# Kernel optimization log

Hardware: AMD Instinct MI355X
Metric: run time of the kernel (lower is better)

## Reference

```python
import jax, jax.numpy as jnp
import numpy as np

B, N, D_IN, D_H, D_OUT = 2, 512, 128, 128, 128


def _mlp2(x, W1, b1, W2, b2):
    # Linear -> SiLU -> Linear
    h = jax.nn.silu(x @ W1 + b1)
    return h @ W2 + b2


def _safe_norm(d2):
    # norm with zero (not NaN) gradient at 0, matching torch.norm's subgradient
    pos = d2 > 0
    return jnp.where(pos, jnp.sqrt(jnp.where(pos, d2, 1.0)), 0.0)


def setup_inputs() -> dict:
    key = jax.random.key(0)
    ks = jax.random.split(key, 16)

    def lin(k, fan_in, fan_out):
        bound = 1.0 / np.sqrt(fan_in)
        kw, kb = jax.random.split(k)
        W = jax.random.uniform(kw, (fan_in, fan_out), jnp.float32, -bound, bound)
        b = jax.random.uniform(kb, (fan_out,), jnp.float32, -bound, bound)
        return W, b

    Ws1, bs1 = lin(ks[0], D_IN, D_H)
    Ws2, bs2 = lin(ks[1], D_H, D_OUT)
    Wv1, bv1 = lin(ks[2], D_IN, D_H)
    Wv2, bv2 = lin(ks[3], D_H, D_OUT)
    Wa1, ba1 = lin(ks[4], D_IN + 3, D_H)
    Wa2, ba2 = lin(ks[5], D_H, 1)

    node_features = jax.random.normal(ks[6], (B, N, D_IN), jnp.float32)
    coordinates = jax.random.normal(ks[7], (B, N, 3), jnp.float32)
    edge_mask = jax.random.randint(ks[8], (B, N, N), 0, 2, jnp.int32)

    return dict(node_features=node_features, coordinates=coordinates, edge_mask=edge_mask,
                Ws1=Ws1, bs1=bs1, Ws2=Ws2, bs2=bs2,
                Wv1=Wv1, bv1=bv1, Wv2=Wv2, bv2=bv2,
                Wa1=Wa1, ba1=ba1, Wa2=Wa2, ba2=ba2)


def reference(node_features, coordinates, edge_mask,
              Ws1, bs1, Ws2, bs2, Wv1, bv1, Wv2, bv2, Wa1, ba1, Wa2, ba2):
    num_atoms = node_features.shape[1]

    # pairwise geometry: diff[b,i,j,:] = x_i - x_j
    diff = coordinates[:, :, None, :] - coordinates[:, None, :, :]  # [B,N,N,3]
    d2 = jnp.sum(diff * diff, axis=-1)
    distances = _safe_norm(d2)  # [B,N,N]

    # per-node scalar branch
    scalar_features = _mlp2(node_features, Ws1, bs1, Ws2, bs2)  # [B,N,D_OUT]

    # radial features + broadcast node features -> attention MLP
    dist_features = jnp.stack(
        [distances, 1.0 / (distances + 1e-6), jnp.exp(-distances)], axis=-1)  # [B,N,N,3]
    nf_exp = jnp.broadcast_to(node_features[:, :, None, :],
                              node_features.shape[:2] + (num_atoms, node_features.shape[-1]))
    attention_input = jnp.concatenate([nf_exp, dist_features], axis=-1)  # [B,N,N,D_IN+3]
    attn_logits = _mlp2(attention_input, Wa1, ba1, Wa2, ba2)[..., 0]  # [B,N,N]

    attn_logits = jnp.where(edge_mask != 0, attn_logits, -jnp.inf)
    attention_weights = jax.nn.softmax(attn_logits, axis=-1)  # [B,N,N]

    # direction-weighted aggregation
    vector_aggregated = jnp.einsum('bijc,bij->bic', diff, attention_weights)  # [B,N,3]

    vector_features = _mlp2(node_features, Wv1, bv1, Wv2, bv2)  # [B,N,D_OUT]
    vector_out = vector_aggregated * vector_features[..., :3]  # [B,N,3]

    return scalar_features, vector_out
```

## Files before the change

kernel.cpp:

```cpp
#include <hip/hip_runtime.h>
#include <math.h>

#define NB 2
#define NN 512
#define DD 128
#define LOG2E 1.4426950408889634f

typedef unsigned long long ull;

__device__ __forceinline__ float exp2_hw(float x) {
    float r; asm("v_exp_f32 %0, %1" : "=v"(r) : "v"(x)); return r;
}
__device__ __forceinline__ float silu_f(float x) {
    float e = exp2_hw(-LOG2E * x);
    return x * __builtin_amdgcn_rcpf(1.0f + e);
}

#define UPD(P, Ae, ff1, ff2, ff3, accv)                                       \
    { float pre = fmaf(ff3, P.w, fmaf(ff2, P.z, fmaf(ff1, P.y, P.x)));        \
      float e   = exp2_hw(pre);                                               \
      float rc  = __builtin_amdgcn_rcpf(1.0f + e);                            \
      accv      = fmaf(pre * Ae, rc, accv); }

__global__ __launch_bounds__(256) void k_all(
    const float* __restrict__ nf,
    const float* __restrict__ coords,
    const int*   __restrict__ mask,
    const float* __restrict__ Ws1, const float* __restrict__ bs1,
    const float* __restrict__ Ws2, const float* __restrict__ bs2,
    const float* __restrict__ Wv1, const float* __restrict__ bv1,
    const float* __restrict__ Wv2, const float* __restrict__ bv2,
    const float* __restrict__ Wa1, const float* __restrict__ ba1,
    const float* __restrict__ Wa2, const float* __restrict__ ba2p,
    float* __restrict__ scalar_out,
    float* __restrict__ vec_out)
{
    __shared__ __align__(16) float s_nf[DD];
    __shared__ __align__(16) float s_hs[DD];
    __shared__ __align__(16) float s_hv[DD];
    __shared__ __align__(16) float s_am[DD];
    __shared__ float  s_part[3][256];
    __shared__ float4 s_pk[DD];
    __shared__ short  s_act[NN];
    __shared__ int    s_cnt8[8], s_off8[8], s_nactS;
    __shared__ float  s_red[4], s_red2[4][4];

    const int row  = blockIdx.x;
    const int b    = row >> 9;
    const int tid  = threadIdx.x;
    const int lane = tid & 63;
    const int wid  = tid >> 6;
    const int c    = tid & 127;
    const int h    = tid >> 7;

    if (tid < DD) s_nf[tid] = nf[row * DD + tid];
    const int* mrow = mask + (size_t)row * NN;
    const bool m0 = (mrow[tid]       != 0);
    const bool m1 = (mrow[tid + 256] != 0);
    const ull  bal0 = __ballot(m0);
    const ull  bal1 = __ballot(m1);
    if (lane == 0) {
        s_cnt8[wid]     = __popcll(bal0);
        s_cnt8[4 + wid] = __popcll(bal1);
    }
    __syncthreads();

    if (tid == 0) {
        int a = 0;
        #pragma unroll
        for (int q = 0; q < 8; ++q) { s_off8[q] = a; a += s_cnt8[q]; }
        s_nactS = a;
    }
    {
        float ps = 0.f, pv = 0.f, pa = 0.f;
        const float4* nf4 = (const float4*)s_nf;
        const int kq0 = h * 16;
        #pragma unroll 4
        for (int kk = 0; kk < 16; ++kk) {
            float4 x = nf4[kq0 + kk];
            const int k = (kq0 + kk) * 4;
            ps = fmaf(x.x, Ws1[(k+0)*DD + c], ps);
            ps = fmaf(x.y, Ws1[(k+1)*DD + c], ps);
            ps = fmaf(x.z, Ws1[(k+2)*DD + c], ps);
            ps = fmaf(x.w, Ws1[(k+3)*DD + c], ps);
            pv = fmaf(x.x, Wv1[(k+0)*DD + c], pv);
            pv = fmaf(x.y, Wv1[(k+1)*DD + c], pv);
            pv = fmaf(x.z, Wv1[(k+2)*DD + c], pv);
            pv = fmaf(x.w, Wv1[(k+3)*DD + c], pv);
            pa = fmaf(x.x, Wa1[(k+0)*DD + c], pa);
            pa = fmaf(x.y, Wa1[(k+1)*DD + c], pa);
            pa = fmaf(x.z, Wa1[(k+2)*DD + c], pa);
            pa = fmaf(x.w, Wa1[(k+3)*DD + c], pa);
        }
        s_part[0][tid] = ps;
        s_part[1][tid] = pv;
        s_part[2][tid] = pa;
    }
    __syncthreads();

    if (tid < DD) {
        s_hs[tid] = silu_f(s_part[0][tid] + s_part[0][128 + tid] + bs1[tid]);
        s_hv[tid] = silu_f(s_part[1][tid] + s_part[1][128 + tid] + bv1[tid]);
        float base = s_part[2][tid] + s_part[2][128 + tid] + ba1[tid];
        float4 p;
        p.x = -LOG2E * base;
        p.y = -LOG2E * Wa1[128 * DD + tid];
        p.z = -LOG2E * Wa1[129 * DD + tid];
        p.w = -LOG2E * Wa1[130 * DD + tid];
        s_pk[tid] = p;
        s_am[tid] = -Wa2[tid];
    }
    {
        const ull lm = (1ull << lane) - 1ull;
        if (m0) s_act[s_off8[wid]     + __popcll(bal0 & lm)] = (short)tid;
        if (m1) s_act[s_off8[4 + wid] + __popcll(bal1 & lm)] = (short)(tid + 256);
    }
    __syncthreads();

    {
        float pb = 0.f;
        const float4* hs4 = (const float4*)s_hs;
        const int kq0 = h * 16;
        #pragma unroll 4
        for (int kk = 0; kk < 16; ++kk) {
            float4 x = hs4[kq0 + kk];
            const int k = (kq0 + kk) * 4;
            pb = fmaf(x.x, Ws2[(k+0)*DD + c], pb);
            pb = fmaf(x.y, Ws2[(k+1)*DD + c], pb);
            pb = fmaf(x.z, Ws2[(k+2)*DD + c], pb);
            pb = fmaf(x.w, Ws2[(k+3)*DD + c], pb);
        }
        s_part[0][tid] = pb;
    }
    if (tid >= 128 && tid < 224) {
        const int idx = tid - 128;
        const int col = idx >> 5;
        const int kq  = idx & 31;
        float vp = 0.f;
        #pragma unroll
        for (int u = 0; u < 4; ++u) {
            const int k = 4 * kq + u;
            vp = fmaf(s_hv[k], Wv2[k * DD + col], vp);
        }
        s_part[1][tid] = vp;
    }

    const int nact = __builtin_amdgcn_readfirstlane(s_nactS);
    const bool act0 = (tid < nact);
    const bool act1 = (tid + 256 < nact);
    const bool w_has1 = ((tid & ~63) + 256) < nact;

    const float ba2l = ba2p[0] * LOG2E;
    const float xi0 = coords[row * 3 + 0];
    const float xi1 = coords[row * 3 + 1];
    const float xi2 = coords[row * 3 + 2];
    const float* cb = coords + (size_t)b * NN * 3;

    float dx0 = 0.f, dy0 = 0.f, dz0 = 0.f, f1_0 = 0.f, f2_0 = 0.f, f3_0 = 0.f;
    float dx1 = 0.f, dy1 = 0.f, dz1 = 0.f, f1_1 = 0.f, f2_1 = 0.f, f3_1 = 0.f;
    float acc0 = ba2l, acc1 = ba2l;

    {
        const int j = ((int)s_act[act0 ? tid : 0]) & (NN - 1);
        dx0 = xi0 - cb[j * 3 + 0];
        dy0 = xi1 - cb[j * 3 + 1];
        dz0 = xi2 - cb[j * 3 + 2];
        float d2 = fmaf(dx0, dx0, fmaf(dy0, dy0, dz0 * dz0));
        float d  = sqrtf(d2);
        f1_0 = d;
        float x  = d + 1e-6f;
        float rc = __builtin_amdgcn_rcpf(x);
        f2_0 = rc * fmaf(-x, rc, 2.0f);
        f3_0 = exp2_hw(-LOG2E * d);
    }
    if (w_has1) {
        const int j = ((int)s_act[act1 ? tid + 256 : 0]) & (NN - 1);
        dx1 = xi0 - cb[j * 3 + 0];
        dy1 = xi1 - cb[j * 3 + 1];
        dz1 = xi2 - cb[j * 3 + 2];
        float d2 = fmaf(dx1, dx1, fmaf(dy1, dy1, dz1 * dz1));
        float d  = sqrtf(d2);
        f1_1 = d;
        float x  = d + 1e-6f;
        float rc = __builtin_amdgcn_rcpf(x);
        f2_1 = rc * fmaf(-x, rc, 2.0f);
        f3_1 = exp2_hw(-LOG2E * d);
    }

    const float4* A4 = (const float4*)s_am;
    for (int t4 = 0; t4 < DD / 4; ++t4) {
        float4 A  = A4[t4];
        float4 P0 = s_pk[4 * t4 + 0];
        float4 P1 = s_pk[4 * t4 + 1];
        float4 P2 = s_pk[4 * t4 + 2];
        float4 P3 = s_pk[4 * t4 + 3];
        UPD(P0, A.x, f1_0, f2_0, f3_0, acc0);
        UPD(P1, A.y, f1_0, f2_0, f3_0, acc0);
        UPD(P2, A.z, f1_0, f2_0, f3_0, acc0);
        UPD(P3, A.w, f1_0, f2_0, f3_0, acc0);
        if (w_has1) {
            UPD(P0, A.x, f1_1, f2_1, f3_1, acc1);
            UPD(P1, A.y, f1_1, f2_1, f3_1, acc1);
            UPD(P2, A.z, f1_1, f2_1, f3_1, acc1);
            UPD(P3, A.w, f1_1, f2_1, f3_1, acc1);
        }
    }
    __syncthreads();

    if (tid < DD) {
        scalar_out[row * DD + tid] = s_part[0][tid] + s_part[0][128 + tid] + bs2[tid];
    }
    float vf_col = 0.f;
    if (tid < 3) {
        float v = bv2[tid];
        const float* pp = &s_part[1][128 + tid * 32];
        for (int r = 0; r < 32; ++r) v += pp[r];
        vf_col = v;
    }

    float mloc = -__builtin_inff();
    if (act0) mloc = acc0;
    if (act1) mloc = fmaxf(mloc, acc1);
    #pragma unroll
    for (int ofs = 32; ofs >= 1; ofs >>= 1) mloc = fmaxf(mloc, __shfl_xor(mloc, ofs));
    if (lane == 0) s_red[wid] = mloc;
    __syncthreads();
    const float mx = fmaxf(fmaxf(s_red[0], s_red[1]), fmaxf(s_red[2], s_red[3]));

    float es = 0.f, wx = 0.f, wy = 0.f, wz = 0.f;
    if (act0) {
        float e = exp2_hw(acc0 - mx);
        es += e; wx = fmaf(e, dx0, wx); wy = fmaf(e, dy0, wy); wz = fmaf(e, dz0, wz);
    }
    if (w_has1 && act1) {
        float e = exp2_hw(acc1 - mx);
        es += e; wx = fmaf(e, dx1, wx); wy = fmaf(e, dy1, wy); wz = fmaf(e, dz1, wz);
    }
    #pragma unroll
    for (int ofs = 32; ofs >= 1; ofs >>= 1) {
        es += __shfl_xor(es, ofs);
        wx += __shfl_xor(wx, ofs);
        wy += __shfl_xor(wy, ofs);
        wz += __shfl_xor(wz, ofs);
    }
    if (lane == 0) {
        s_red2[wid][0] = es; s_red2[wid][1] = wx;
        s_red2[wid][2] = wy; s_red2[wid][3] = wz;
    }
    __syncthreads();

    if (tid < 3) {
        float tot = s_red2[0][0] + s_red2[1][0] + s_red2[2][0] + s_red2[3][0];
        float num = s_red2[0][1+tid] + s_red2[1][1+tid] + s_red2[2][1+tid] + s_red2[3][1+tid];
        vec_out[row * 3 + tid] = (num / tot) * vf_col;
    }
}

extern "C" void kernel_launch(void* const* d_in, const int* in_sizes, int n_in,
                              void* d_out, int out_size, void* d_ws, size_t ws_size,
                              hipStream_t stream) {
    const float* nf     = (const float*)d_in[0];
    const float* coords = (const float*)d_in[1];
    const int*   mask   = (const int*)  d_in[2];
    const float* Ws1 = (const float*)d_in[3];  const float* bs1 = (const float*)d_in[4];
    const float* Ws2 = (const float*)d_in[5];  const float* bs2 = (const float*)d_in[6];
    const float* Wv1 = (const float*)d_in[7];  const float* bv1 = (const float*)d_in[8];
    const float* Wv2 = (const float*)d_in[9];  const float* bv2 = (const float*)d_in[10];
    const float* Wa1 = (const float*)d_in[11]; const float* ba1 = (const float*)d_in[12];
    const float* Wa2 = (const float*)d_in[13]; const float* ba2 = (const float*)d_in[14];

    float* scalar_out = (float*)d_out;
    float* vec_out    = (float*)d_out + NB * NN * DD;

    hipLaunchKernelGGL(k_all, dim3(NB * NN), dim3(256), 0, stream,
                       nf, coords, mask,
                       Ws1, bs1, Ws2, bs2, Wv1, bv1, Wv2, bv2,
                       Wa1, ba1, Wa2, ba2,
                       scalar_out, vec_out);
}
```

Before: 27.83 us.

## Process two rows per block to reuse weight loads and shared tables

Each block now handles two query rows instead of one, halving the grid to 512 blocks. Every weight element loaded from global memory in the node MLPs feeds two accumulators, and each shared-memory Wa1 tail/Wa2 entry read in the attention loop serves both rows. The per-row bias is split out of the packed float4 into a separate per-row array. This cuts redundant weight traffic and per-block fixed overhead, at the cost of more registers per thread and fewer blocks to spread across CUs.

```diff
diff --git a/kernel.cpp b/kernel.cpp
--- a/kernel.cpp
+++ b/kernel.cpp
@@ -16,11 +16,11 @@
     return x * __builtin_amdgcn_rcpf(1.0f + e);
 }
 
-#define UPD(P, Ae, ff1, ff2, ff3, accv)                                       \
-    { float pre = fmaf(ff3, P.w, fmaf(ff2, P.z, fmaf(ff1, P.y, P.x)));        \
-      float e   = exp2_hw(pre);                                               \
-      float rc  = __builtin_amdgcn_rcpf(1.0f + e);                            \
-      accv      = fmaf(pre * Ae, rc, accv); }
+#define UPD(Wq, bbv, s)                                                        \
+    { float pre = fmaf(f3[s], Wq.z, fmaf(f2[s], Wq.y, fmaf(f1[s], Wq.x, bbv))); \
+      float e   = exp2_hw(pre);                                                \
+      float rc  = __builtin_amdgcn_rcpf(1.0f + e);                             \
+      acc[s]    = fmaf(pre * Wq.w, rc, acc[s]); }
 
 __global__ __launch_bounds__(256) void k_all(
     const float* __restrict__ nf,
@@ -35,224 +35,262 @@
     float* __restrict__ scalar_out,
     float* __restrict__ vec_out)
 {
-    __shared__ __align__(16) float s_nf[DD];
-    __shared__ __align__(16) float s_hs[DD];
-    __shared__ __align__(16) float s_hv[DD];
-    __shared__ __align__(16) float s_am[DD];
-    __shared__ float  s_part[3][256];
-    __shared__ float4 s_pk[DD];
-    __shared__ short  s_act[NN];
-    __shared__ int    s_cnt8[8], s_off8[8], s_nactS;
-    __shared__ float  s_red[4], s_red2[4][4];
-
-    const int row  = blockIdx.x;
-    const int b    = row >> 9;
+    __shared__ __align__(16) float  s_nf[2][DD];
+    __shared__ __align__(16) float  s_hs[2][DD];
+    __shared__ __align__(16) float  s_hv[2][DD];
+    __shared__ __align__(16) float  s_bb[2][DD];
+    __shared__ __align__(16) float4 s_w4[DD];
+    __shared__ float  s_part[3][2][256];
+    __shared__ short  s_act[2][NN];
+    __shared__ int    s_cnt8[2][8], s_off8[2][8], s_nact[2];
+    __shared__ float  s_red[2][4], s_red2[2][4][4];
+
+    const int row0 = blockIdx.x * 2;
+    const int b    = row0 >> 9;
     const int tid  = threadIdx.x;
     const int lane = tid & 63;
     const int wid  = tid >> 6;
     const int c    = tid & 127;
     const int h    = tid >> 7;
 
-    if (tid < DD) s_nf[tid] = nf[row * DD + tid];
-    const int* mrow = mask + (size_t)row * NN;
-    const bool m0 = (mrow[tid]       != 0);
-    const bool m1 = (mrow[tid + 256] != 0);
-    const ull  bal0 = __ballot(m0);
-    const ull  bal1 = __ballot(m1);
+    { const int rr = tid >> 7, t = tid & 127;
+      s_nf[rr][t] = nf[(row0 + rr) * DD + t]; }
+
+    const int* mrow0 = mask + (size_t)row0 * NN;
+    const int* mrow1 = mrow0 + NN;
+    const bool m00 = (mrow0[tid] != 0), m01 = (mrow0[tid + 256] != 0);
+    const bool m10 = (mrow1[tid] != 0), m11 = (mrow1[tid + 256] != 0);
+    const ull  b00 = __ballot(m00), b01 = __ballot(m01);
+    const ull  b10 = __ballot(m10), b11 = __ballot(m11);
     if (lane == 0) {
-        s_cnt8[wid]     = __popcll(bal0);
-        s_cnt8[4 + wid] = __popcll(bal1);
-    }
-    __syncthreads();
-
-    if (tid == 0) {
+        s_cnt8[0][wid]     = __popcll(b00);
+        s_cnt8[0][4 + wid] = __popcll(b01);
+        s_cnt8[1][wid]     = __popcll(b10);
+        s_cnt8[1][4 + wid] = __popcll(b11);
+    }
+    __syncthreads();
+
+    if (tid < 2) {
         int a = 0;
         #pragma unroll
-        for (int q = 0; q < 8; ++q) { s_off8[q] = a; a += s_cnt8[q]; }
-        s_nactS = a;
-    }
-    {
-        float ps = 0.f, pv = 0.f, pa = 0.f;
-        const float4* nf4 = (const float4*)s_nf;
+        for (int q = 0; q < 8; ++q) { s_off8[tid][q] = a; a += s_cnt8[tid][q]; }
+        s_nact[tid] = a;
+    }
+
+    {
+        float pS0 = 0.f, pS1 = 0.f, pV0 = 0.f, pV1 = 0.f, pA0 = 0.f, pA1 = 0.f;
+        const float4* nfq0 = (const float4*)s_nf[0];
+        const float4* nfq1 = (const float4*)s_nf[1];
         const int kq0 = h * 16;
         #pragma unroll 4
         for (int kk = 0; kk < 16; ++kk) {
-            float4 x = nf4[kq0 + kk];
+            float4 x0 = nfq0[kq0 + kk];
+            float4 x1 = nfq1[kq0 + kk];
             const int k = (kq0 + kk) * 4;
-            ps = fmaf(x.x, Ws1[(k+0)*DD + c], ps);
-            ps = fmaf(x.y, Ws1[(k+1)*DD + c], ps);
-            ps = fmaf(x.z, Ws1[(k+2)*DD + c], ps);
-            ps = fmaf(x.w, Ws1[(k+3)*DD + c], ps);
-            pv = fmaf(x.x, Wv1[(k+0)*DD + c], pv);
-            pv = fmaf(x.y, Wv1[(k+1)*DD + c], pv);
-            pv = fmaf(x.z, Wv1[(k+2)*DD + c], pv);
-            pv = fmaf(x.w, Wv1[(k+3)*DD + c], pv);
-            pa = fmaf(x.x, Wa1[(k+0)*DD + c], pa);
-            pa = fmaf(x.y, Wa1[(k+1)*DD + c], pa);
-            pa = fmaf(x.z, Wa1[(k+2)*DD + c], pa);
-            pa = fmaf(x.w, Wa1[(k+3)*DD + c], pa);
-        }
-        s_part[0][tid] = ps;
-        s_part[1][tid] = pv;
-        s_part[2][tid] = pa;
-    }
-    __syncthreads();
-
+            float w;
+            w = Ws1[(k+0)*DD + c]; pS0 = fmaf(x0.x, w, pS0); pS1 = fmaf(x1.x, w, pS1);
+            w = Ws1[(k+1)*DD + c]; pS0 = fmaf(x0.y, w, pS0); pS1 = fmaf(x1.y, w, pS1);
+            w = Ws1[(k+2)*DD + c]; pS0 = fmaf(x0.z, w, pS0); pS1 = fmaf(x1.z, w, pS1);
+            w = Ws1[(k+3)*DD + c]; pS0 = fmaf(x0.w, w, pS0); pS1 = fmaf(x1.w, w, pS1);
+            w = Wv1[(k+0)*DD + c]; pV0 = fmaf(x0.x, w, pV0); pV1 = fmaf(x1.x, w, pV1);
+            w = Wv1[(k+1)*DD + c]; pV0 = fmaf(x0.y, w, pV0); pV1 = fmaf(x1.y, w, pV1);
+            w = Wv1[(k+2)*DD + c]; pV0 = fmaf(x0.z, w, pV0); pV1 = fmaf(x1.z, w, pV1);
+            w = Wv1[(k+3)*DD + c]; pV0 = fmaf(x0.w, w, pV0); pV1 = fmaf(x1.w, w, pV1);
+            w = Wa1[(k+0)*DD + c]; pA0 = fmaf(x0.x, w, pA0); pA1 = fmaf(x1.x, w, pA1);
+            w = Wa1[(k+1)*DD + c]; pA0 = fmaf(x0.y, w, pA0); pA1 = fmaf(x1.y, w, pA1);
+            w = Wa1[(k+2)*DD + c]; pA0 = fmaf(x0.z, w, pA0); pA1 = fmaf(x1.z, w, pA1);
+            w = Wa1[(k+3)*DD + c]; pA0 = fmaf(x0.w, w, pA0); pA1 = fmaf(x1.w, w, pA1);
+        }
+        s_part[0][0][tid] = pS0; s_part[0][1][tid] = pS1;
+        s_part[1][0][tid] = pV0; s_part[1][1][tid] = pV1;
+        s_part[2][0][tid] = pA0; s_part[2][1][tid] = pA1;
+    }
+    __syncthreads();
+
+    {
+        const int rr = tid >> 7, t = tid & 127;
+        s_hs[rr][t] = silu_f(s_part[0][rr][t] + s_part[0][rr][128 + t] + bs1[t]);
+        s_hv[rr][t] = silu_f(s_part[1][rr][t] + s_part[1][rr][128 + t] + bv1[t]);
+        s_bb[rr][t] = -LOG2E * (s_part[2][rr][t] + s_part[2][rr][128 + t] + ba1[t]);
+    }
     if (tid < DD) {
-        s_hs[tid] = silu_f(s_part[0][tid] + s_part[0][128 + tid] + bs1[tid]);
-        s_hv[tid] = silu_f(s_part[1][tid] + s_part[1][128 + tid] + bv1[tid]);
-        float base = s_part[2][tid] + s_part[2][128 + tid] + ba1[tid];
-        float4 p;
-        p.x = -LOG2E * base;
-        p.y = -LOG2E * Wa1[128 * DD + tid];
-        p.z = -LOG2E * Wa1[129 * DD + tid];
-        p.w = -LOG2E * Wa1[130 * DD + tid];
-        s_pk[tid] = p;
-        s_am[tid] = -Wa2[tid];
+        float4 w;
+        w.x = -LOG2E * Wa1[128 * DD + tid];
+        w.y = -LOG2E * Wa1[129 * DD + tid];
+        w.z = -LOG2E * Wa1[130 * DD + tid];
+        w.w = -Wa2[tid];
+        s_w4[tid] = w;
     }
     {
         const ull lm = (1ull << lane) - 1ull;
-        if (m0) s_act[s_off8[wid]     + __popcll(bal0 & lm)] = (short)tid;
-        if (m1) s_act[s_off8[4 + wid] + __popcll(bal1 & lm)] = (short)(tid + 256);
-    }
-    __syncthreads();
-
-    {
-        float pb = 0.f;
-        const float4* hs4 = (const float4*)s_hs;
+        if (m00) s_act[0][s_off8[0][wid]     + __popcll(b00 & lm)] = (short)tid;
+        if (m01) s_act[0][s_off8[0][4 + wid] + __popcll(b01 & lm)] = (short)(tid + 256);
+        if (m10) s_act[1][s_off8[1][wid]     + __popcll(b10 & lm)] = (short)tid;
+        if (m11) s_act[1][s_off8[1][4 + wid] + __popcll(b11 & lm)] = (short)(tid + 256);
+    }
+    __syncthreads();
+
+    {
+        float p0 = 0.f, p1 = 0.f;
+        const float4* h0 = (const float4*)s_hs[0];
+        const float4* h1 = (const float4*)s_hs[1];
         const int kq0 = h * 16;
         #pragma unroll 4
         for (int kk = 0; kk < 16; ++kk) {
-            float4 x = hs4[kq0 + kk];
+            float4 x0 = h0[kq0 + kk];
+            float4 x1 = h1[kq0 + kk];
             const int k = (kq0 + kk) * 4;
-            pb = fmaf(x.x, Ws2[(k+0)*DD + c], pb);
-            pb = fmaf(x.y, Ws2[(k+1)*DD + c], pb);
-            pb = fmaf(x.z, Ws2[(k+2)*DD + c], pb);
-            pb = fmaf(x.w, Ws2[(k+3)*DD + c], pb);
-        }
-        s_part[0][tid] = pb;
-    }
-    if (tid >= 128 && tid < 224) {
-        const int idx = tid - 128;
-        const int col = idx >> 5;
-        const int kq  = idx & 31;
+            float w;
+            w = Ws2[(k+0)*DD + c]; p0 = fmaf(x0.x, w, p0); p1 = fmaf(x1.x, w, p1);
+            w = Ws2[(k+1)*DD + c]; p0 = fmaf(x0.y, w, p0); p1 = fmaf(x1.y, w, p1);
+            w = Ws2[(k+2)*DD + c]; p0 = fmaf(x0.z, w, p0); p1 = fmaf(x1.z, w, p1);
+            w = Ws2[(k+3)*DD + c]; p0 = fmaf(x0.w, w, p0); p1 = fmaf(x1.w, w, p1);
+        }
+        s_part[0][0][tid] = p0; s_part[0][1][tid] = p1;
+    }
+    float* vfp = &s_part[1][0][0];
+    if (tid < 192) {
+        const int rr  = tid / 96;
+        const int rem = tid % 96;
+        const int col = rem >> 5;
+        const int kq  = rem & 31;
         float vp = 0.f;
         #pragma unroll
         for (int u = 0; u < 4; ++u) {
             const int k = 4 * kq + u;
-            vp = fmaf(s_hv[k], Wv2[k * DD + col], vp);
-        }
-        s_part[1][tid] = vp;
-    }
-
-    const int nact = __builtin_amdgcn_readfirstlane(s_nactS);
-    const bool act0 = (tid < nact);
-    const bool act1 = (tid + 256 < nact);
-    const bool w_has1 = ((tid & ~63) + 256) < nact;
+            vp = fmaf(s_hv[rr][k], Wv2[k * DD + col], vp);
+        }
+        vfp[tid] = vp;
+    }
+
+    const int n0 = __builtin_amdgcn_readfirstlane(s_nact[0]);
+    const int n1 = __builtin_amdgcn_readfirstlane(s_nact[1]);
+    const int wb = (tid & ~63) + 256;
+    const bool has1r0 = wb < n0;
+    const bool has1r1 = wb < n1;
+    bool act[4];
+    act[0] = tid < n0;  act[1] = tid + 256 < n0;
+    act[2] = tid < n1;  act[3] = tid + 256 < n1;
 
     const float ba2l = ba2p[0] * LOG2E;
-    const float xi0 = coords[row * 3 + 0];
-    const float xi1 = coords[row * 3 + 1];
-    const float xi2 = coords[row * 3 + 2];
+    float xi[2][3];
+    #pragma unroll
+    for (int rr = 0; rr < 2; ++rr)
+        #pragma unroll
+        for (int cc = 0; cc < 3; ++cc) xi[rr][cc] = coords[(row0 + rr) * 3 + cc];
     const float* cb = coords + (size_t)b * NN * 3;
 
-    float dx0 = 0.f, dy0 = 0.f, dz0 = 0.f, f1_0 = 0.f, f2_0 = 0.f, f3_0 = 0.f;
-    float dx1 = 0.f, dy1 = 0.f, dz1 = 0.f, f1_1 = 0.f, f2_1 = 0.f, f3_1 = 0.f;
-    float acc0 = ba2l, acc1 = ba2l;
-
-    {
-        const int j = ((int)s_act[act0 ? tid : 0]) & (NN - 1);
-        dx0 = xi0 - cb[j * 3 + 0];
-        dy0 = xi1 - cb[j * 3 + 1];
-        dz0 = xi2 - cb[j * 3 + 2];
-        float d2 = fmaf(dx0, dx0, fmaf(dy0, dy0, dz0 * dz0));
+    float dx[4], dy[4], dz[4], f1[4], f2[4], f3[4], acc[4];
+    #pragma unroll
+    for (int s = 0; s < 4; ++s) {
+        acc[s] = ba2l;
+        dx[s] = dy[s] = dz[s] = f1[s] = f2[s] = f3[s] = 0.f;
+    }
+    #pragma unroll
+    for (int s = 0; s < 4; ++s) {
+        const int rr = s >> 1;
+        const bool rnd1 = (s & 1);
+        if (rnd1 && !(rr == 0 ? has1r0 : has1r1)) continue;
+        const int a = tid + (rnd1 ? 256 : 0);
+        const int j = ((int)s_act[rr][act[s] ? a : 0]) & (NN - 1);
+        dx[s] = xi[rr][0] - cb[j * 3 + 0];
+        dy[s] = xi[rr][1] - cb[j * 3 + 1];
+        dz[s] = xi[rr][2] - cb[j * 3 + 2];
+        float d2 = fmaf(dx[s], dx[s], fmaf(dy[s], dy[s], dz[s] * dz[s]));
         float d  = sqrtf(d2);
-        f1_0 = d;
+        f1[s] = d;
         float x  = d + 1e-6f;
         float rc = __builtin_amdgcn_rcpf(x);
-        f2_0 = rc * fmaf(-x, rc, 2.0f);
-        f3_0 = exp2_hw(-LOG2E * d);
-    }
-    if (w_has1) {
-        const int j = ((int)s_act[act1 ? tid + 256 : 0]) & (NN - 1);
-        dx1 = xi0 - cb[j * 3 + 0];
-        dy1 = xi1 - cb[j * 3 + 1];
-        dz1 = xi2 - cb[j * 3 + 2];
-        float d2 = fmaf(dx1, dx1, fmaf(dy1, dy1, dz1 * dz1));
-        float d  = sqrtf(d2);
-        f1_1 = d;
-        float x  = d + 1e-6f;
-        float rc = __builtin_amdgcn_rcpf(x);
-        f2_1 = rc * fmaf(-x, rc, 2.0f);
-        f3_1 = exp2_hw(-LOG2E * d);
-    }
-
-    const float4* A4 = (const float4*)s_am;
+        f2[s] = rc * fmaf(-x, rc, 2.0f);
+        f3[s] = exp2_hw(-LOG2E * d);
+    }
+
+    const float4* bbq0 = (const float4*)s_bb[0];
+    const float4* bbq1 = (const float4*)s_bb[1];
     for (int t4 = 0; t4 < DD / 4; ++t4) {
-        float4 A  = A4[t4];
-        float4 P0 = s_pk[4 * t4 + 0];
-        float4 P1 = s_pk[4 * t4 + 1];
-        float4 P2 = s_pk[4 * t4 + 2];
-        float4 P3 = s_pk[4 * t4 + 3];
-        UPD(P0, A.x, f1_0, f2_0, f3_0, acc0);
-        UPD(P1, A.y, f1_0, f2_0, f3_0, acc0);
-        UPD(P2, A.z, f1_0, f2_0, f3_0, acc0);
-        UPD(P3, A.w, f1_0, f2_0, f3_0, acc0);
-        if (w_has1) {
-            UPD(P0, A.x, f1_1, f2_1, f3_1, acc1);
-            UPD(P1, A.y, f1_1, f2_1, f3_1, acc1);
-            UPD(P2, A.z, f1_1, f2_1, f3_1, acc1);
-            UPD(P3, A.w, f1_1, f2_1, f3_1, acc1);
-        }
-    }
-    __syncthreads();
-
-    if (tid < DD) {
-        scalar_out[row * DD + tid] = s_part[0][tid] + s_part[0][128 + tid] + bs2[tid];
-    }
-    float vf_col = 0.f;
-    if (tid < 3) {
-        float v = bv2[tid];
-        const float* pp = &s_part[1][128 + tid * 32];
-        for (int r = 0; r < 32; ++r) v += pp[r];
-        vf_col = v;
-    }
-
-    float mloc = -__builtin_inff();
-    if (act0) mloc = acc0;
-    if (act1) mloc = fmaxf(mloc, acc1);
-    #pragma unroll
-    for (int ofs = 32; ofs >= 1; ofs >>= 1) mloc = fmaxf(mloc, __shfl_xor(mloc, ofs));
-    if (lane == 0) s_red[wid] = mloc;
-    __syncthreads();
-    const float mx = fmaxf(fmaxf(s_red[0], s_red[1]), fmaxf(s_red[2], s_red[3]));
-
-    float es = 0.f, wx = 0.f, wy = 0.f, wz = 0.f;
-    if (act0) {
-        float e = exp2_hw(acc0 - mx);
-        es += e; wx = fmaf(e, dx0, wx); wy = fmaf(e, dy0, wy); wz = fmaf(e, dz0, wz);
-    }
-    if (w_has1 && act1) {
-        float e = exp2_hw(acc1 - mx);
-        es += e; wx = fmaf(e, dx1, wx); wy = fmaf(e, dy1, wy); wz = fmaf(e, dz1, wz);
-    }
+        float4 W0 = s_w4[4 * t4 + 0];
+        float4 W1 = s_w4[4 * t4 + 1];
+        float4 W2 = s_w4[4 * t4 + 2];
+        float4 W3 = s_w4[4 * t4 + 3];
+        float4 bA = bbq0[t4];
+        float4 bB = bbq1[t4];
+        UPD(W0, bA.x, 0); UPD(W1, bA.y, 0); UPD(W2, bA.z, 0); UPD(W3, bA.w, 0);
+        UPD(W0, bB.x, 2); UPD(W1, bB.y, 2); UPD(W2, bB.z, 2); UPD(W3, bB.w, 2);
+        if (has1r0) {
+            UPD(W0, bA.x, 1); UPD(W1, bA.y, 1); UPD(W2, bA.z, 1); UPD(W3, bA.w, 1);
+        }
+        if (has1r1) {
+            UPD(W0, bB.x, 3); UPD(W1, bB.y, 3); UPD(W2, bB.z, 3); UPD(W3, bB.w, 3);
+        }
+    }
+    __syncthreads();
+
+    {
+        const int rr = tid >> 7, t = tid & 127;
+        scalar_out[(row0 + rr) * DD + t] =
+            s_part[0][rr][t] + s_part[0][rr][128 + t] + bs2[t];
+    }
+
+    float mloc[2] = { -__builtin_inff(), -__builtin_inff() };
+    if (act[0]) mloc[0] = acc[0];
+    if (has1r0 && act[1]) mloc[0] = fmaxf(mloc[0], acc[1]);
+    if (act[2]) mloc[1] = acc[2];
+    if (has1r1 && act[3]) mloc[1] = fmaxf(mloc[1], acc[3]);
     #pragma unroll
     for (int ofs = 32; ofs >= 1; ofs >>= 1) {
-        es += __shfl_xor(es, ofs);
-        wx += __shfl_xor(wx, ofs);
-        wy += __shfl_xor(wy, ofs);
-        wz += __shfl_xor(wz, ofs);
+        mloc[0] = fmaxf(mloc[0], __shfl_xor(mloc[0], ofs));
+        mloc[1] = fmaxf(mloc[1], __shfl_xor(mloc[1], ofs));
+    }
+    if (lane == 0) { s_red[0][wid] = mloc[0]; s_red[1][wid] = mloc[1]; }
+    __syncthreads();
+    const float mx0 = fmaxf(fmaxf(s_red[0][0], s_red[0][1]), fmaxf(s_red[0][2], s_red[0][3]));
+    const float mx1 = fmaxf(fmaxf(s_red[1][0], s_red[1][1]), fmaxf(s_red[1][2], s_red[1][3]));
+
+    float es[2] = {0.f, 0.f}, wx[2] = {0.f, 0.f}, wy[2] = {0.f, 0.f}, wz[2] = {0.f, 0.f};
+    if (act[0]) {
+        float e = exp2_hw(acc[0] - mx0);
+        es[0] += e; wx[0] = fmaf(e, dx[0], wx[0]); wy[0] = fmaf(e, dy[0], wy[0]); wz[0] = fmaf(e, dz[0], wz[0]);
+    }
+    if (has1r0 && act[1]) {
+        float e = exp2_hw(acc[1] - mx0);
+        es[0] += e; wx[0] = fmaf(e, dx[1], wx[0]); wy[0] = fmaf(e, dy[1], wy[0]); wz[0] = fmaf(e, dz[1], wz[0]);
+    }
+    if (act[2]) {
+        float e = exp2_hw(acc[2] - mx1);
+        es[1] += e; wx[1] = fmaf(e, dx[2], wx[1]); wy[1] = fmaf(e, dy[2], wy[1]); wz[1] = fmaf(e, dz[2], wz[1]);
+    }
+    if (has1r1 && act[3]) {
+        float e = exp2_hw(acc[3] - mx1);
+        es[1] += e; wx[1] = fmaf(e, dx[3], wx[1]); wy[1] = fmaf(e, dy[3], wy[1]); wz[1] = fmaf(e, dz[3], wz[1]);
+    }
+    #pragma unroll
+    for (int ofs = 32; ofs >= 1; ofs >>= 1) {
+        #pragma unroll
+        for (int rr = 0; rr < 2; ++rr) {
+            es[rr] += __shfl_xor(es[rr], ofs);
+            wx[rr] += __shfl_xor(wx[rr], ofs);
+            wy[rr] += __shfl_xor(wy[rr], ofs);
+            wz[rr] += __shfl_xor(wz[rr], ofs);
+        }
     }
     if (lane == 0) {
-        s_red2[wid][0] = es; s_red2[wid][1] = wx;
-        s_red2[wid][2] = wy; s_red2[wid][3] = wz;
-    }
-    __syncthreads();
-
-    if (tid < 3) {
-        float tot = s_red2[0][0] + s_red2[1][0] + s_red2[2][0] + s_red2[3][0];
-        float num = s_red2[0][1+tid] + s_red2[1][1+tid] + s_red2[2][1+tid] + s_red2[3][1+tid];
-        vec_out[row * 3 + tid] = (num / tot) * vf_col;
+        #pragma unroll
+        for (int rr = 0; rr < 2; ++rr) {
+            s_red2[rr][wid][0] = es[rr]; s_red2[rr][wid][1] = wx[rr];
+            s_red2[rr][wid][2] = wy[rr]; s_red2[rr][wid][3] = wz[rr];
+        }
+    }
+    __syncthreads();
+
+    if (tid < 6) {
+        const int rr = tid / 3, cc = tid % 3;
+        float tot = s_red2[rr][0][0] + s_red2[rr][1][0] + s_red2[rr][2][0] + s_red2[rr][3][0];
+        float num = s_red2[rr][0][1+cc] + s_red2[rr][1][1+cc] + s_red2[rr][2][1+cc] + s_red2[rr][3][1+cc];
+        float vf = bv2[cc];
+        const float* pp = &vfp[rr * 96 + cc * 32];
+        #pragma unroll 8
+        for (int q = 0; q < 32; ++q) vf += pp[q];
+        vec_out[(row0 + rr) * 3 + cc] = (num / tot) * vf;
     }
 }
 
@@ -272,7 +310,7 @@
     float* scalar_out = (float*)d_out;
     float* vec_out    = (float*)d_out + NB * NN * DD;
 
-    hipLaunchKernelGGL(k_all, dim3(NB * NN), dim3(256), 0, stream,
+    hipLaunchKernelGGL(k_all, dim3(NB * NN / 2), dim3(256), 0, stream,
                        nf, coords, mask,
                        Ws1, bs1, Ws2, bs2, Wv1, bv1, Wv2, bv2,
                        Wa1, ba1, Wa2, ba2,
```

After: 29.05 us. 1.04x slower.
